# Performance work log

Measured on AMD Instinct MI355X. Metric: run time of the kernel, lower is better.

The kernel has to match this reference:

```python
import jax, jax.numpy as jnp
import numpy as np

H, C = 5, 64            # attention heads, per-head channels (out_channels=conv_dim)
NEG_SLOPE = 0.2         # GATv2 leaky_relu slope
N_NODES = 50000

def setup_inputs() -> dict:
    key = jax.random.key(0)
    ks = jax.random.split(key, 10)
    N, E = N_NODES, 400000
    node_dim, edge_dim = 128, 16
    s = 0.1
    return {
        'x': jax.random.normal(ks[0], (N, node_dim), jnp.float32),
        'edge_index': jax.random.randint(ks[1], (2, E), 0, N),
        'edge_attr': jax.random.normal(ks[2], (E, edge_dim), jnp.float32),
        'W0': jax.random.normal(ks[3], (node_dim, H * C), jnp.float32) * s,
        'b0': jnp.zeros((H * C,), jnp.float32),
        'We0': jax.random.normal(ks[4], (edge_dim, H * C), jnp.float32) * s,
        'att0': jax.random.normal(ks[5], (H, C), jnp.float32) * s,
        'bias0': jnp.zeros((C,), jnp.float32),
        'W12': jax.random.normal(ks[6], (2, C, H * C), jnp.float32) * s,
        'b12': jnp.zeros((2, H * C), jnp.float32),
        'We12': jax.random.normal(ks[7], (2, edge_dim, H * C), jnp.float32) * s,
        'att12': jax.random.normal(ks[8], (2, H, C), jnp.float32) * s,
        'bias12': jnp.zeros((2, C), jnp.float32),
    }

def _add_self_loops_mean(edge_index, edge_attr, N):
    # PyG add_self_loops(fill_value='mean'): self-loop attr = mean of incoming edge attrs per dst node
    dst = edge_index[1]
    sums = jax.ops.segment_sum(edge_attr, dst, num_segments=N)
    cnt = jax.ops.segment_sum(jnp.ones((edge_attr.shape[0], 1), edge_attr.dtype), dst, num_segments=N)
    loop_attr = sums / jnp.maximum(cnt, 1.0)
    loop = jnp.arange(N, dtype=edge_index.dtype)
    ei = jnp.concatenate([edge_index, jnp.stack([loop, loop])], axis=1)
    ea = jnp.concatenate([edge_attr, loop_attr], axis=0)
    return ei, ea

def _gatv2_layer(x, src, dst, eattr, W, b, We, att, bias, N):
    h = (x @ W + b).reshape(N, H, C)                     # shared lin_l==lin_r (share_weights=True)
    e = (eattr @ We).reshape(-1, H, C)                   # lin_edge (no bias)
    s = jax.nn.leaky_relu(h[src] + h[dst] + e, NEG_SLOPE)  # [E', H, C]
    logits = jnp.einsum('ehc,hc->eh', s, att)            # [E', H]
    m = jax.ops.segment_max(logits, dst, num_segments=N)
    m = jnp.where(jnp.isfinite(m), m, 0.0)
    ex = jnp.exp(logits - m[dst])
    denom = jax.ops.segment_sum(ex, dst, num_segments=N) + 1e-16
    alpha = ex / denom[dst]                              # per-dst softmax (dropout off: eval mode)
    msg = h[src] * alpha[:, :, None]
    out = jax.ops.segment_sum(msg, dst, num_segments=N)  # [N, H, C]
    return out.mean(axis=1) + bias                       # concat=False -> head mean, then bias

def reference(x, edge_index, edge_attr, W0, b0, We0, att0, bias0, W12, b12, We12, att12, bias12):
    N = x.shape[0]
    ei, ea = _add_self_loops_mean(edge_index, edge_attr, N)
    src, dst = ei[0], ei[1]
    h = jax.nn.elu(_gatv2_layer(x, src, dst, ea, W0, b0, We0, att0, bias0, N))
    for i in range(2):
        h = jax.nn.elu(_gatv2_layer(h, src, dst, ea, W12[i], b12[i], We12[i], att12[i], bias12[i], N))
    return h  # jk_mode='last'
```

## Files before the change

### kernel.cpp

```cpp
#include <hip/hip_runtime.h>
#include <hip/hip_fp16.h>
#include <math.h>

#define NH 5
#define NC 64
#define ED 16
#define HC 320
#define HP 8
#define CH 32

typedef _Float16 h2  __attribute__((ext_vector_type(2)));
typedef _Float16 v8h __attribute__((ext_vector_type(8)));
typedef float    v4f __attribute__((ext_vector_type(4)));

template<int ctrl, int rmask>
__device__ __forceinline__ float dpp_add(float x) {
    int y = __builtin_amdgcn_update_dpp(0, __float_as_int(x), ctrl, rmask, 0xf, true);
    return x + __int_as_float(y);
}
__device__ __forceinline__ float wave_sum_all(float x) {
    x = dpp_add<0xb1, 0xf>(x);
    x = dpp_add<0x4e, 0xf>(x);
    x = dpp_add<0x114, 0xf>(x);
    x = dpp_add<0x118, 0xf>(x);
    x = dpp_add<0x142, 0xa>(x);
    x = dpp_add<0x143, 0xc>(x);
    return __int_as_float(__builtin_amdgcn_readlane(__float_as_int(x), 63));
}


__global__ void count_kernel(const int* __restrict__ dst, int* __restrict__ cnt, int E) {
    int t = blockIdx.x * blockDim.x + threadIdx.x;
    if (t >= E) return;
    atomicAdd(&cnt[dst[t]], 1);
}

__global__ void scan_kernel(const int* __restrict__ cnt, int* __restrict__ offsets,
                            int* __restrict__ cursor, int N) {
    __shared__ int sums[1024];
    int t = threadIdx.x;
    int chunk = (N + 1023) / 1024;
    int beg = t * chunk;
    int end = min(beg + chunk, N);
    int s = 0;
    for (int i = beg; i < end; ++i) s += cnt[i] + 1;
    sums[t] = s;
    __syncthreads();
    for (int o = 1; o < 1024; o <<= 1) {
        int v = (t >= o) ? sums[t - o] : 0;
        __syncthreads();
        sums[t] += v;
        __syncthreads();
    }
    int run = (t > 0) ? sums[t - 1] : 0;
    for (int i = beg; i < end; ++i) {
        offsets[i] = run; cursor[i] = run;
        run += cnt[i] + 1;
    }
    if (t == 0) offsets[N] = sums[1023];
}

__global__ void scatter_kernel(const int* __restrict__ src, const int* __restrict__ dst,
                               int* __restrict__ cursor, int2* __restrict__ recs, int N, int E) {
    int t = blockIdx.x * blockDim.x + threadIdx.x;
    if (t >= E + N) return;
    int d, s;
    if (t < E) { d = dst[t]; s = src[t]; }
    else       { d = t - E; s = t - E; }
    int pos = atomicAdd(&cursor[d], 1);
    recs[pos] = make_int2(s, t);
}

__global__ void loop_from_csr(const int* __restrict__ offsets, const int2* __restrict__ recs,
                              const float* __restrict__ ea, float* __restrict__ loop,
                              int N, int E) {
    int t = blockIdx.x * blockDim.x + threadIdx.x;
    int n = t >> 4, k = t & 15;
    if (n >= N) return;
    int beg = offsets[n], end = offsets[n + 1];
    float s = 0.f; int c = 0;
    for (int j = beg; j < end; ++j) {
        int y = recs[j].y;
        if (y < E) { s += ea[(size_t)y * ED + k]; ++c; }
    }
    loop[(size_t)n * ED + k] = s / (float)max(c, 1);
}

__global__ void reorder_ea(const int2* __restrict__ recs, const float* __restrict__ ea,
                           const float* __restrict__ loop, h2* __restrict__ easrt,
                           int R, int E) {
    int t = blockIdx.x * blockDim.x + threadIdx.x;
    int slot = t >> 3, k2 = t & 7;
    if (slot >= R) return;
    int y = recs[slot].y;
    const float2* sp = (const float2*)((y < E) ? ea + (size_t)y * ED : loop + (size_t)(y - E) * ED);
    float2 f = sp[k2];
    h2 o; o.x = (_Float16)f.x; o.y = (_Float16)f.y;
    easrt[(size_t)slot * 8 + k2] = o;
}

__global__ void win_start_kernel(const int* __restrict__ offsets, int* __restrict__ winStart, int N) {
    int i = blockIdx.x * blockDim.x + threadIdx.x;
    if (i >= N) return;
    atomicMin(&winStart[offsets[i] / CH], i);
}

__global__ void cvt_f16(const float* __restrict__ in, _Float16* __restrict__ out, int n) {
    int i = blockIdx.x * blockDim.x + threadIdx.x;
    if (i < n) out[i] = (_Float16)in[i];
}

__global__ void transpose_w(const float* __restrict__ W, _Float16* __restrict__ Wt, int K) {
    int t = blockIdx.x * blockDim.x + threadIdx.x;
    if (t >= 320 * K) return;
    int k = t / 320, n = t % 320;
    Wt[(size_t)n * K + k] = (_Float16)W[t];
}

__global__ __launch_bounds__(256) void gemm_mfma(const _Float16* __restrict__ A,
                                                 const _Float16* __restrict__ Bt,
                                                 const float* __restrict__ bias,
                                                 _Float16* __restrict__ Cout, int M, int K) {
    __shared__ _Float16 lds[4][8][NC * HP];
    int lane = threadIdx.x & 63;
    int wave = threadIdx.x >> 6;
    int m = lane & 15, quad = lane >> 4;
    int rowBase = (blockIdx.x * 4 + wave) * 16;
    bool active = rowBase < M;

    v4f acc[20];
#pragma unroll
    for (int c = 0; c < 20; ++c) acc[c] = (v4f){0.f, 0.f, 0.f, 0.f};

    if (active) {
        for (int k0 = 0; k0 < K; k0 += 32) {
            v8h a = *(const v8h*)&A[(size_t)(rowBase + m) * K + k0 + quad * 8];
#pragma unroll
            for (int c = 0; c < 20; ++c) {
                v8h b = *(const v8h*)&Bt[(size_t)(c * 16 + m) * K + k0 + quad * 8];
                acc[c] = __builtin_amdgcn_mfma_f32_16x16x32_f16(a, b, acc[c], 0, 0, 0);
            }
        }
    }
#pragma unroll
    for (int pass = 0; pass < 2; ++pass) {
        if (active && (quad >> 1) == pass) {
#pragma unroll
            for (int c = 0; c < 20; ++c) {
                int cc = c * 16 + m;
                int idx = (cc & 63) * HP + (cc >> 6);
                float bb = bias[cc];
#pragma unroll
                for (int r = 0; r < 4; ++r)
                    lds[wave][(quad & 1) * 4 + r][idx] = (_Float16)(acc[c][r] + bb);
            }
        }
        __syncthreads();
        if (active) {
#pragma unroll
            for (int rr = 0; rr < 8; ++rr) {
                v8h v = *(const v8h*)&lds[wave][rr][lane * HP];
                *(v8h*)&Cout[(size_t)(rowBase + pass * 8 + rr) * (NC * HP) + lane * HP] = v;
            }
        }
        __syncthreads();
    }
}

__global__ __launch_bounds__(256) void gat_fused(const _Float16* __restrict__ hbuf,
                                                 const int* __restrict__ offsets,
                                                 const int2* __restrict__ recs,
                                                 const h2* __restrict__ easrt,
                                                 const int* __restrict__ winStart,
                                                 const float* __restrict__ We,
                                                 const float* __restrict__ att,
                                                 const float* __restrict__ bias,
                                                 _Float16* __restrict__ outH,
                                                 float* __restrict__ outF,
                                                 int N, int R) {
    int lane = threadIdx.x & 63;
    int wave = (blockIdx.x * blockDim.x + threadIdx.x) >> 6;
    int totalWaves = (gridDim.x * blockDim.x) >> 6;

    h2 we2[8 * NH];
#pragma unroll
    for (int k2 = 0; k2 < 8; ++k2)
#pragma unroll
        for (int h = 0; h < NH; ++h) {
            h2 w;
            w.x = (_Float16)We[(2 * k2) * HC + h * NC + lane];
            w.y = (_Float16)We[(2 * k2 + 1) * HC + h * NC + lane];
            we2[k2 * NH + h] = w;
        }
    const float L2E = 1.4426950408889634f;
    float attc6[NH], attc4[NH];
#pragma unroll
    for (int h = 0; h < NH; ++h) {
        float a = att[h * NC + lane];
        attc6[h] = 0.6f * a * L2E;
        attc4[h] = 0.4f * a * L2E;
    }
    float bc = bias[lane];

    for (int w = wave; w * CH < R; w += totalWaves) {
        int i = winStart[w];
        if (i >= N) continue;
        int winEnd = w * CH + CH;
        for (; i < N; ++i) {
            int beg = offsets[i];
            if (beg >= winEnd) break;
            int end = offsets[i + 1];

            v8h hdv = *(const v8h*)&hbuf[(size_t)i * (NC * HP) + lane * HP];
            float hd[NH];
#pragma unroll
            for (int h = 0; h < NH; ++h) hd[h] = (float)hdv[h];

            float l[NH] = {}, acc[NH] = {};
            for (int t = beg; t < end; ++t) {
                int tu = __builtin_amdgcn_readfirstlane(t);
                int src = recs[tu].x;
                const h2* ap = easrt + (size_t)tu * 8;
                h2 a[8];
#pragma unroll
                for (int k2 = 0; k2 < 8; ++k2) a[k2] = ap[k2];
                v8h hsv = *(const v8h*)&hbuf[(size_t)src * (NC * HP) + lane * HP];
                float hs[NH];
#pragma unroll
                for (int h = 0; h < NH; ++h) hs[h] = (float)hsv[h];

                float p[NH];
#pragma unroll
                for (int h = 0; h < NH; ++h) {
                    float v = hs[h] + hd[h];
#pragma unroll
                    for (int k2 = 0; k2 < 8; ++k2)
                        v = __builtin_amdgcn_fdot2(a[k2], we2[k2 * NH + h], v, false);
                    p[h] = fmaf(fabsf(v), attc4[h], v * attc6[h]);
                }
#pragma unroll
                for (int h = 0; h < NH; ++h) {
                    float pe = exp2f(wave_sum_all(p[h]));
                    l[h] += pe;
                    acc[h] = fmaf(pe, hs[h], acc[h]);
                }
            }
            float o = 0.f;
#pragma unroll
            for (int h = 0; h < NH; ++h) o += acc[h] / l[h];
            o = o * 0.2f + bc;
            o = o > 0.f ? o : expm1f(o);
            if (outF) outF[(size_t)i * NC + lane] = o;
            else      outH[(size_t)i * NC + lane] = (_Float16)o;
        }
    }
}

extern "C" void kernel_launch(void* const* d_in, const int* in_sizes, int n_in,
                              void* d_out, int out_size, void* d_ws, size_t ws_size,
                              hipStream_t stream) {
    const float* x     = (const float*)d_in[0];
    const int*   ei    = (const int*)d_in[1];
    const float* ea    = (const float*)d_in[2];
    const float* W0    = (const float*)d_in[3];
    const float* b0    = (const float*)d_in[4];
    const float* We0   = (const float*)d_in[5];
    const float* att0  = (const float*)d_in[6];
    const float* bias0 = (const float*)d_in[7];
    const float* W12   = (const float*)d_in[8];
    const float* b12   = (const float*)d_in[9];
    const float* We12  = (const float*)d_in[10];
    const float* att12 = (const float*)d_in[11];
    const float* bias12= (const float*)d_in[12];

    int N = in_sizes[0] / 128;
    int E = in_sizes[1] / 2;
    int R = E + N;
    int numWin = (R + CH - 1) / CH;
    const int* srcArr = ei;
    const int* dstArr = ei + E;

    char* ws = (char*)d_ws;
    size_t off = 0;
    auto alloc = [&](size_t bytes) -> void* {
        void* p = ws + off;
        off = (off + bytes + 255) & ~(size_t)255;
        return p;
    };
    int*      cnt     = (int*)alloc((size_t)N * 4);
    int*      offsets = (int*)alloc((size_t)(N + 1) * 4);
    int*      cursor  = (int*)alloc((size_t)N * 4);
    int2*     recs    = (int2*)alloc((size_t)R * 8);
    float*    loop    = (float*)alloc((size_t)N * ED * 4);
    _Float16* hbuf    = (_Float16*)alloc((size_t)N * NC * HP * 2);
    _Float16* acth    = (_Float16*)alloc((size_t)N * NC * 2);
    _Float16* xh      = (_Float16*)alloc((size_t)N * 128 * 2);
    _Float16* Wth0    = (_Float16*)alloc((size_t)320 * 128 * 2);
    _Float16* Wth1    = (_Float16*)alloc((size_t)320 * 64 * 2);
    _Float16* Wth2    = (_Float16*)alloc((size_t)320 * 64 * 2);
    int*      winStart= (int*)alloc((size_t)(numWin + 1) * 4);
    h2*       easrt   = (h2*)alloc((size_t)R * 32);

    (void)hipMemsetAsync(cnt, 0, (size_t)N * 4, stream);
    (void)hipMemsetAsync(winStart, 0x7f, (size_t)(numWin + 1) * 4, stream);
    count_kernel<<<(E + 255) / 256, 256, 0, stream>>>(dstArr, cnt, E);
    scan_kernel<<<1, 1024, 0, stream>>>(cnt, offsets, cursor, N);
    scatter_kernel<<<(E + N + 255) / 256, 256, 0, stream>>>(srcArr, dstArr, cursor, recs, N, E);
    loop_from_csr<<<((size_t)N * ED + 255) / 256, 256, 0, stream>>>(offsets, recs, ea, loop, N, E);
    reorder_ea<<<((size_t)R * 8 + 255) / 256, 256, 0, stream>>>(recs, ea, loop, easrt, R, E);
    win_start_kernel<<<(N + 255) / 256, 256, 0, stream>>>(offsets, winStart, N);
    cvt_f16<<<((size_t)N * 128 + 255) / 256, 256, 0, stream>>>(x, xh, N * 128);
    transpose_w<<<(320 * 128 + 255) / 256, 256, 0, stream>>>(W0, Wth0, 128);
    transpose_w<<<(320 * 64 + 255) / 256, 256, 0, stream>>>(W12, Wth1, 64);
    transpose_w<<<(320 * 64 + 255) / 256, 256, 0, stream>>>(W12 + 64 * HC, Wth2, 64);

    float* dout = (float*)d_out;
    int gemmBlocks = (N / 16 + 3) / 4 + 1;
    int fusedBlocks = 2048;

    const _Float16* As[3]  = {xh, acth, acth};
    const _Float16* Bts[3] = {Wth0, Wth1, Wth2};
    int Ks[3] = {128, 64, 64};
    const float* bs[3]   = {b0, b12, b12 + HC};
    const float* Wes[3]  = {We0, We12, We12 + ED * HC};
    const float* atts[3] = {att0, att12, att12 + NH * NC};
    const float* bis[3]  = {bias0, bias12, bias12 + NC};
    for (int layer = 0; layer < 3; ++layer) {
        gemm_mfma<<<gemmBlocks, 256, 0, stream>>>(As[layer], Bts[layer], bs[layer], hbuf, N, Ks[layer]);
        gat_fused<<<fusedBlocks, 256, 0, stream>>>(hbuf, offsets, recs, easrt, winStart,
                                                   Wes[layer], atts[layer], bis[layer],
                                                   acth, (layer == 2) ? dout : nullptr, N, R);
    }
}
```

Baseline: 876.2 us.

## Fuse x fp16 conversion into layer-0 GEMM and size GAT windows per wave

Removes the separate fp32-to-fp16 conversion kernel by converting x inside the layer-0 MFMA GEMM through a templated A-load path. Replaces the fixed 32-record windows and grid-stride loop in the GAT kernel with a window size computed so each wave processes exactly one window (about 8192 windows total). This cuts a full pass over x plus a kernel launch, and removes the loop and redundant per-iteration setup. In exchange, windows become larger and fixed per wave, which may change load balance.

```diff
diff --git a/kernel.cpp b/kernel.cpp
--- a/kernel.cpp
+++ b/kernel.cpp
@@ -7,7 +7,6 @@
 #define ED 16
 #define HC 320
 #define HP 8
-#define CH 32
 
 typedef _Float16 h2  __attribute__((ext_vector_type(2)));
 typedef _Float16 v8h __attribute__((ext_vector_type(8)));
@@ -99,15 +98,11 @@
     easrt[(size_t)slot * 8 + k2] = o;
 }
 
-__global__ void win_start_kernel(const int* __restrict__ offsets, int* __restrict__ winStart, int N) {
+__global__ void win_start_kernel(const int* __restrict__ offsets, int* __restrict__ winStart,
+                                 int N, int CHw) {
     int i = blockIdx.x * blockDim.x + threadIdx.x;
     if (i >= N) return;
-    atomicMin(&winStart[offsets[i] / CH], i);
-}
-
-__global__ void cvt_f16(const float* __restrict__ in, _Float16* __restrict__ out, int n) {
-    int i = blockIdx.x * blockDim.x + threadIdx.x;
-    if (i < n) out[i] = (_Float16)in[i];
+    atomicMin(&winStart[offsets[i] / CHw], i);
 }
 
 __global__ void transpose_w(const float* __restrict__ W, _Float16* __restrict__ Wt, int K) {
@@ -117,7 +112,8 @@
     Wt[(size_t)n * K + k] = (_Float16)W[t];
 }
 
-__global__ __launch_bounds__(256) void gemm_mfma(const _Float16* __restrict__ A,
+template<bool F32A>
+__global__ __launch_bounds__(256) void gemm_mfma(const void* __restrict__ Araw,
                                                  const _Float16* __restrict__ Bt,
                                                  const float* __restrict__ bias,
                                                  _Float16* __restrict__ Cout, int M, int K) {
@@ -134,7 +130,18 @@
 
     if (active) {
         for (int k0 = 0; k0 < K; k0 += 32) {
-            v8h a = *(const v8h*)&A[(size_t)(rowBase + m) * K + k0 + quad * 8];
+            v8h a;
+            if (F32A) {
+                const float* ap = (const float*)Araw + (size_t)(rowBase + m) * K + k0 + quad * 8;
+                float4 f0 = *(const float4*)ap;
+                float4 f1 = *(const float4*)(ap + 4);
+                a[0] = (_Float16)f0.x; a[1] = (_Float16)f0.y;
+                a[2] = (_Float16)f0.z; a[3] = (_Float16)f0.w;
+                a[4] = (_Float16)f1.x; a[5] = (_Float16)f1.y;
+                a[6] = (_Float16)f1.z; a[7] = (_Float16)f1.w;
+            } else {
+                a = *(const v8h*)((const _Float16*)Araw + (size_t)(rowBase + m) * K + k0 + quad * 8);
+            }
 #pragma unroll
             for (int c = 0; c < 20; ++c) {
                 v8h b = *(const v8h*)&Bt[(size_t)(c * 16 + m) * K + k0 + quad * 8];
@@ -177,20 +184,23 @@
                                                  const float* __restrict__ bias,
                                                  _Float16* __restrict__ outH,
                                                  float* __restrict__ outF,
-                                                 int N, int R) {
+                                                 int N, int R, int CHw) {
     int lane = threadIdx.x & 63;
-    int wave = (blockIdx.x * blockDim.x + threadIdx.x) >> 6;
-    int totalWaves = (gridDim.x * blockDim.x) >> 6;
+    int w = (blockIdx.x * blockDim.x + threadIdx.x) >> 6;
+    if (w * CHw >= R) return;
+    int i = winStart[w];
+    if (i >= N) return;
+    int winEnd = w * CHw + CHw;
 
     h2 we2[8 * NH];
 #pragma unroll
     for (int k2 = 0; k2 < 8; ++k2)
 #pragma unroll
         for (int h = 0; h < NH; ++h) {
-            h2 w;
-            w.x = (_Float16)We[(2 * k2) * HC + h * NC + lane];
-            w.y = (_Float16)We[(2 * k2 + 1) * HC + h * NC + lane];
-            we2[k2 * NH + h] = w;
+            h2 wv;
+            wv.x = (_Float16)We[(2 * k2) * HC + h * NC + lane];
+            wv.y = (_Float16)We[(2 * k2 + 1) * HC + h * NC + lane];
+            we2[k2 * NH + h] = wv;
         }
     const float L2E = 1.4426950408889634f;
     float attc6[NH], attc4[NH];
@@ -202,57 +212,52 @@
     }
     float bc = bias[lane];
 
-    for (int w = wave; w * CH < R; w += totalWaves) {
-        int i = winStart[w];
-        if (i >= N) continue;
-        int winEnd = w * CH + CH;
-        for (; i < N; ++i) {
-            int beg = offsets[i];
-            if (beg >= winEnd) break;
-            int end = offsets[i + 1];
-
-            v8h hdv = *(const v8h*)&hbuf[(size_t)i * (NC * HP) + lane * HP];
-            float hd[NH];
-#pragma unroll
-            for (int h = 0; h < NH; ++h) hd[h] = (float)hdv[h];
-
-            float l[NH] = {}, acc[NH] = {};
-            for (int t = beg; t < end; ++t) {
-                int tu = __builtin_amdgcn_readfirstlane(t);
-                int src = recs[tu].x;
-                const h2* ap = easrt + (size_t)tu * 8;
-                h2 a[8];
-#pragma unroll
-                for (int k2 = 0; k2 < 8; ++k2) a[k2] = ap[k2];
-                v8h hsv = *(const v8h*)&hbuf[(size_t)src * (NC * HP) + lane * HP];
-                float hs[NH];
-#pragma unroll
-                for (int h = 0; h < NH; ++h) hs[h] = (float)hsv[h];
-
-                float p[NH];
-#pragma unroll
-                for (int h = 0; h < NH; ++h) {
-                    float v = hs[h] + hd[h];
-#pragma unroll
-                    for (int k2 = 0; k2 < 8; ++k2)
-                        v = __builtin_amdgcn_fdot2(a[k2], we2[k2 * NH + h], v, false);
-                    p[h] = fmaf(fabsf(v), attc4[h], v * attc6[h]);
-                }
-#pragma unroll
-                for (int h = 0; h < NH; ++h) {
-                    float pe = exp2f(wave_sum_all(p[h]));
-                    l[h] += pe;
-                    acc[h] = fmaf(pe, hs[h], acc[h]);
-                }
-            }
-            float o = 0.f;
-#pragma unroll
-            for (int h = 0; h < NH; ++h) o += acc[h] / l[h];
-            o = o * 0.2f + bc;
-            o = o > 0.f ? o : expm1f(o);
-            if (outF) outF[(size_t)i * NC + lane] = o;
-            else      outH[(size_t)i * NC + lane] = (_Float16)o;
-        }
+    for (; i < N; ++i) {
+        int beg = offsets[i];
+        if (beg >= winEnd) break;
+        int end = offsets[i + 1];
+
+        v8h hdv = *(const v8h*)&hbuf[(size_t)i * (NC * HP) + lane * HP];
+        float hd[NH];
+#pragma unroll
+        for (int h = 0; h < NH; ++h) hd[h] = (float)hdv[h];
+
+        float l[NH] = {}, acc[NH] = {};
+        for (int t = beg; t < end; ++t) {
+            int tu = __builtin_amdgcn_readfirstlane(t);
+            int src = recs[tu].x;
+            const h2* ap = easrt + (size_t)tu * 8;
+            h2 a[8];
+#pragma unroll
+            for (int k2 = 0; k2 < 8; ++k2) a[k2] = ap[k2];
+            v8h hsv = *(const v8h*)&hbuf[(size_t)src * (NC * HP) + lane * HP];
+            float hs[NH];
+#pragma unroll
+            for (int h = 0; h < NH; ++h) hs[h] = (float)hsv[h];
+
+            float p[NH];
+#pragma unroll
+            for (int h = 0; h < NH; ++h) {
+                float v = hs[h] + hd[h];
+#pragma unroll
+                for (int k2 = 0; k2 < 8; ++k2)
+                    v = __builtin_amdgcn_fdot2(a[k2], we2[k2 * NH + h], v, false);
+                p[h] = fmaf(fabsf(v), attc4[h], v * attc6[h]);
+            }
+#pragma unroll
+            for (int h = 0; h < NH; ++h) {
+                float pe = exp2f(wave_sum_all(p[h]));
+                l[h] += pe;
+                acc[h] = fmaf(pe, hs[h], acc[h]);
+            }
+        }
+        float o = 0.f;
+#pragma unroll
+        for (int h = 0; h < NH; ++h) o += acc[h] / l[h];
+        o = o * 0.2f + bc;
+        o = o > 0.f ? o : expm1f(o);
+        if (outF) outF[(size_t)i * NC + lane] = o;
+        else      outH[(size_t)i * NC + lane] = (_Float16)o;
     }
 }
 
@@ -276,7 +281,8 @@
     int N = in_sizes[0] / 128;
     int E = in_sizes[1] / 2;
     int R = E + N;
-    int numWin = (R + CH - 1) / CH;
+    int CHw = (R + 8191) / 8192;
+    int numWin = (R + CHw - 1) / CHw;
     const int* srcArr = ei;
     const int* dstArr = ei + E;
 
@@ -294,7 +300,6 @@
     float*    loop    = (float*)alloc((size_t)N * ED * 4);
     _Float16* hbuf    = (_Float16*)alloc((size_t)N * NC * HP * 2);
     _Float16* acth    = (_Float16*)alloc((size_t)N * NC * 2);
-    _Float16* xh      = (_Float16*)alloc((size_t)N * 128 * 2);
     _Float16* Wth0    = (_Float16*)alloc((size_t)320 * 128 * 2);
     _Float16* Wth1    = (_Float16*)alloc((size_t)320 * 64 * 2);
     _Float16* Wth2    = (_Float16*)alloc((size_t)320 * 64 * 2);
@@ -308,17 +313,15 @@
     scatter_kernel<<<(E + N + 255) / 256, 256, 0, stream>>>(srcArr, dstArr, cursor, recs, N, E);
     loop_from_csr<<<((size_t)N * ED + 255) / 256, 256, 0, stream>>>(offsets, recs, ea, loop, N, E);
     reorder_ea<<<((size_t)R * 8 + 255) / 256, 256, 0, stream>>>(recs, ea, loop, easrt, R, E);
-    win_start_kernel<<<(N + 255) / 256, 256, 0, stream>>>(offsets, winStart, N);
-    cvt_f16<<<((size_t)N * 128 + 255) / 256, 256, 0, stream>>>(x, xh, N * 128);
+    win_start_kernel<<<(N + 255) / 256, 256, 0, stream>>>(offsets, winStart, N, CHw);
     transpose_w<<<(320 * 128 + 255) / 256, 256, 0, stream>>>(W0, Wth0, 128);
     transpose_w<<<(320 * 64 + 255) / 256, 256, 0, stream>>>(W12, Wth1, 64);
     transpose_w<<<(320 * 64 + 255) / 256, 256, 0, stream>>>(W12 + 64 * HC, Wth2, 64);
 
     float* dout = (float*)d_out;
     int gemmBlocks = (N / 16 + 3) / 4 + 1;
-    int fusedBlocks = 2048;
-
-    const _Float16* As[3]  = {xh, acth, acth};
+    int fusedBlocks = (numWin + 3) / 4;
+
     const _Float16* Bts[3] = {Wth0, Wth1, Wth2};
     int Ks[3] = {128, 64, 64};
     const float* bs[3]   = {b0, b12, b12 + HC};
@@ -326,9 +329,12 @@
     const float* atts[3] = {att0, att12, att12 + NH * NC};
     const float* bis[3]  = {bias0, bias12, bias12 + NC};
     for (int layer = 0; layer < 3; ++layer) {
-        gemm_mfma<<<gemmBlocks, 256, 0, stream>>>(As[layer], Bts[layer], bs[layer], hbuf, N, Ks[layer]);
+        if (layer == 0)
+            gemm_mfma<true><<<gemmBlocks, 256, 0, stream>>>(x, Bts[0], bs[0], hbuf, N, Ks[0]);
+        else
+            gemm_mfma<false><<<gemmBlocks, 256, 0, stream>>>(acth, Bts[layer], bs[layer], hbuf, N, Ks[layer]);
         gat_fused<<<fusedBlocks, 256, 0, stream>>>(hbuf, offsets, recs, easrt, winStart,
                                                    Wes[layer], atts[layer], bis[layer],
-                                                   acth, (layer == 2) ? dout : nullptr, N, R);
-    }
-}
+                                                   acth, (layer == 2) ? dout : nullptr, N, R, CHw);
+    }
+}
```

Result: no change. 882.9 us (+0.8%).
